# Performance work log

Measured on AMD Instinct MI355X. Metric: run time of the kernel, lower is better.

The kernel has to match this reference:

```python
import jax, jax.numpy as jnp
import numpy as np

# Static multi-level feature-map geometry (h, w) per level.
SPATIAL_SHAPES = np.array([[92, 92], [46, 46], [23, 23], [12, 12]], dtype=np.int32)
_AREAS = SPATIAL_SHAPES[:, 0] * SPATIAL_SHAPES[:, 1]
LEVEL_START = np.concatenate([[0], np.cumsum(_AREAS)[:-1]]).astype(np.int32)
LEN_IN = int(_AREAS.sum())  # 11253
N_HEADS, N_LEVELS, N_POINTS = 8, 4, 4
D_MODEL, D_HEAD = 256, 64


def setup_inputs() -> dict:
    key = jax.random.key(0)
    ks = jax.random.split(key, 12)
    N, Lq = 4, 1000
    s = 0.02
    f32 = jnp.float32
    return {
        'query': jax.random.normal(ks[0], (N, Lq, D_MODEL), f32),
        'reference_points': jax.random.uniform(ks[1], (N, Lq, N_LEVELS, 2), f32),
        'input_flatten': jax.random.normal(ks[2], (N, LEN_IN, D_MODEL), f32),
        'input_spatial_shapes': jnp.asarray(SPATIAL_SHAPES),
        'input_level_start_index': jnp.asarray(LEVEL_START),
        'W_off': jax.random.normal(ks[3], (N_HEADS * N_LEVELS * N_POINTS * 2, D_MODEL), f32) * s,
        'b_off': jax.random.normal(ks[4], (N_HEADS * N_LEVELS * N_POINTS * 2,), f32) * 0.5,
        'W_attn': jax.random.normal(ks[5], (N_HEADS * N_LEVELS * N_POINTS, D_MODEL), f32) * s,
        'b_attn': jax.random.normal(ks[6], (N_HEADS * N_LEVELS * N_POINTS,), f32) * s,
        'W_val': jax.random.normal(ks[7], (N_HEADS * D_HEAD, D_MODEL), f32) * s,
        'b_val': jnp.zeros((N_HEADS * D_HEAD,), f32),
        'W_out': jax.random.normal(ks[8], (D_MODEL, N_HEADS * D_HEAD), f32) * s,
        'b_out': jnp.zeros((D_MODEL,), f32),
    }


def _ms_deform_attn(value, sampling_locations, attention_weights):
    # value: [N, Len_in, H, D]; locations: [N, Lq, H, L, P, 2] in [0,1];
    # weights: [N, Lq, H, L, P] -> out [N, Lq, H*D]
    N, _, H, D = value.shape
    Lq, L, P = sampling_locations.shape[1], sampling_locations.shape[3], sampling_locations.shape[4]
    out = jnp.zeros((N, H, Lq, D), value.dtype)
    for l in range(L):
        h, w = int(SPATIAL_SHAPES[l, 0]), int(SPATIAL_SHAPES[l, 1])
        st = int(LEVEL_START[l])
        # per-level value as [N*H, h*w, D]
        v = value[:, st:st + h * w].transpose(0, 2, 1, 3).reshape(N * H, h * w, D)
        loc = sampling_locations[:, :, :, l].transpose(0, 2, 1, 3, 4).reshape(N * H, Lq * P, 2)
        aw = attention_weights[:, :, :, l].transpose(0, 2, 1, 3).reshape(N * H, Lq * P)
        # grid_sample align_corners=False convention (matches CUDA kernel)
        x = loc[..., 0] * w - 0.5
        y = loc[..., 1] * h - 0.5
        x0 = jnp.floor(x)
        y0 = jnp.floor(y)
        lx, ly = x - x0, y - y0
        x0i = x0.astype(jnp.int32)
        y0i = y0.astype(jnp.int32)

        def gather(yi, xi):
            valid = ((xi >= 0) & (xi < w) & (yi >= 0) & (yi < h)).astype(v.dtype)
            idx = jnp.clip(yi, 0, h - 1) * w + jnp.clip(xi, 0, w - 1)
            g = jnp.take_along_axis(v, idx[..., None], axis=1)  # [N*H, Lq*P, D]
            return g * valid[..., None]

        sampled = (gather(y0i, x0i) * ((1 - lx) * (1 - ly))[..., None]
                   + gather(y0i, x0i + 1) * (lx * (1 - ly))[..., None]
                   + gather(y0i + 1, x0i) * ((1 - lx) * ly)[..., None]
                   + gather(y0i + 1, x0i + 1) * (lx * ly)[..., None])
        out = out + (sampled * aw[..., None]).reshape(N, H, Lq, P, D).sum(axis=3)
    return out.transpose(0, 2, 1, 3).reshape(N, Lq, H * D)


def reference(query, reference_points, input_flatten, input_spatial_shapes,
              input_level_start_index, W_off, b_off, W_attn, b_attn,
              W_val, b_val, W_out, b_out):
    N, Lq, _ = query.shape
    Lin = input_flatten.shape[1]
    H, L, P, D = N_HEADS, N_LEVELS, N_POINTS, D_HEAD
    value = (input_flatten @ W_val.T + b_val).reshape(N, Lin, H, D)
    off = (query @ W_off.T + b_off).reshape(N, Lq, H, L, P, 2)
    aw = jax.nn.softmax((query @ W_attn.T + b_attn).reshape(N, Lq, H, L * P), axis=-1)
    aw = aw.reshape(N, Lq, H, L, P)
    # offset normalizer is (w, h) per level
    norm = jnp.asarray(SPATIAL_SHAPES[:, ::-1].copy(), jnp.float32)  # [L, 2]
    loc = reference_points[:, :, None, :, None, :] + off / norm[None, None, None, :, None, :]
    out = _ms_deform_attn(value, loc, aw)
    return out @ W_out.T + b_out
```

## Files before the change

### kernel.cpp

```cpp
#include <hip/hip_runtime.h>


typedef __attribute__((ext_vector_type(4))) float f32x4;
typedef __attribute__((ext_vector_type(8))) short bf16x8;
typedef __attribute__((ext_vector_type(4))) short bf16x4;

static __device__ __forceinline__ unsigned short f2bf(float f) {
    unsigned u = __builtin_bit_cast(unsigned, f);
    u += 0x7FFFu + ((u >> 16) & 1u);
    return (unsigned short)(u >> 16);
}
static __device__ __forceinline__ float bflo(unsigned d) {
    return __builtin_bit_cast(float, d << 16);
}
static __device__ __forceinline__ float bfhi(unsigned d) {
    return __builtin_bit_cast(float, d & 0xffff0000u);
}
static __device__ __forceinline__ void gload_lds16(const void* g, void* l) {
    __builtin_amdgcn_global_load_lds(
        (const __attribute__((address_space(1))) void*)g,
        (__attribute__((address_space(3))) void*)l, 16, 0, 0);
}

__global__ __launch_bounds__(256)
void cvt_k(const float* __restrict__ s0, const float* __restrict__ s1,
           const float* __restrict__ s2, const float* __restrict__ s3,
           const float* __restrict__ s4, const float* __restrict__ s5,
           unsigned short* __restrict__ dst) {
    const size_t i8 = ((size_t)blockIdx.x * 256 + threadIdx.x) * 8;
    if (i8 >= 12907520u) return;
    const float* sp; size_t loc;
    if (i8 < 11523072u)      { sp = s0; loc = i8; }
    else if (i8 < 12547072u) { sp = s1; loc = i8 - 11523072u; }
    else if (i8 < 12612608u) { sp = s2; loc = i8 - 12547072u; }
    else if (i8 < 12645376u) { sp = s3; loc = i8 - 12612608u; }
    else if (i8 < 12776448u) { sp = s4; loc = i8 - 12645376u; }
    else                     { sp = s5; loc = i8 - 12776448u; }
    f32x4 a = *(const f32x4*)(sp + loc);
    f32x4 b = *(const f32x4*)(sp + loc + 4);
    bf16x8 r;
    r[0] = f2bf(a[0]); r[1] = f2bf(a[1]); r[2] = f2bf(a[2]); r[3] = f2bf(a[3]);
    r[4] = f2bf(b[0]); r[5] = f2bf(b[1]); r[6] = f2bf(b[2]); r[7] = f2bf(b[3]);
    *(bf16x8*)(dst + i8) = r;
}

template<int MODE>
__global__ __launch_bounds__(256)
void gemm_bf16_tn(const unsigned short* __restrict__ A,
                  const unsigned short* __restrict__ B,
                  const float* __restrict__ bias, const float* __restrict__ bias2,
                  void* __restrict__ Cv, int M, int N, int K) {
    __shared__ __align__(16) char smem[65536];

    const int tid = threadIdx.x, lane = tid & 63, w = tid >> 6;
    const int wm = w >> 1, wn = w & 1;
    const int bm = blockIdx.x, bn = blockIdx.y;

    const int r8 = lane >> 3;
    const int colsrc = (((lane & 7) ^ r8) << 4);
    const char* pa[4]; const char* pb[4];
#pragma unroll
    for (int j = 0; j < 4; j++) {
        int ra = bm * 128 + j * 32 + w * 8 + r8; ra = ra < M ? ra : M - 1;
        int rb = bn * 128 + j * 32 + w * 8 + r8; rb = rb < N ? rb : N - 1;
        pa[j] = (const char*)A + (size_t)ra * ((size_t)K * 2) + colsrc;
        pb[j] = (const char*)B + (size_t)rb * ((size_t)K * 2) + colsrc;
    }
    const int ldso = w << 10;
    const int NT = K >> 6;

    f32x4 acc[4][4] = {};
    const int fr = lane & 15, fq = lane >> 4;
    const int k8b = fq << 4;
    const int swzR = (fr & 7) << 4;

#pragma unroll
    for (int j = 0; j < 4; j++) {
        gload_lds16(pa[j], smem + j * 4096 + ldso);
        gload_lds16(pb[j], smem + 16384 + j * 4096 + ldso);
    }
    __syncthreads();

    for (int t = 0; t < NT; ++t) {
        const int cur = (t & 1) << 15;
        if (t + 1 < NT) {
            const int nxt = ((t + 1) & 1) << 15;
            const int off = (t + 1) << 7;
#pragma unroll
            for (int j = 0; j < 4; j++) {
                gload_lds16(pa[j] + off, smem + nxt + j * 4096 + ldso);
                gload_lds16(pb[j] + off, smem + nxt + 16384 + j * 4096 + ldso);
            }
        }
#pragma unroll
        for (int kk = 0; kk < 2; ++kk) {
            const int ko = ((kk << 6) + k8b) ^ swzR;
            bf16x8 af[4], bv[4];
#pragma unroll
            for (int m = 0; m < 4; m++)
                af[m] = *(const bf16x8*)(smem + cur + ((wm * 64 + m * 16 + fr) << 7) + ko);
#pragma unroll
            for (int nn = 0; nn < 4; nn++)
                bv[nn] = *(const bf16x8*)(smem + cur + 16384 + ((wn * 64 + nn * 16 + fr) << 7) + ko);
#pragma unroll
            for (int m = 0; m < 4; m++)
#pragma unroll
                for (int nn = 0; nn < 4; nn++)
                    acc[m][nn] = __builtin_amdgcn_mfma_f32_16x16x32_bf16(
                        af[m], bv[nn], acc[m][nn], 0, 0, 0);
        }
        __syncthreads();
    }

    if (MODE != 1) {
        float* C = (float*)Cv;
        const int crow0 = bm * 128 + wm * 64 + fq * 4;
        const int ccol0 = bn * 128 + wn * 64 + fr;
#pragma unroll
        for (int m = 0; m < 4; m++) {
#pragma unroll
            for (int nn = 0; nn < 4; nn++) {
                const int col = ccol0 + nn * 16;
                const float bv2 = (MODE == 2 && col >= 256) ? bias2[col - 256]
                                                            : bias[col];
#pragma unroll
                for (int j = 0; j < 4; j++) {
                    const int row = crow0 + m * 16 + j;
                    if (row < M) C[(size_t)row * N + col] = acc[m][nn][j] + bv2;
                }
            }
        }
    } else {
        unsigned short* tile = (unsigned short*)smem + (size_t)w * (64 * 68);
        const int hh = bn * 2 + wn;
        float bvs[4];
#pragma unroll
        for (int nn = 0; nn < 4; nn++) bvs[nn] = bias[hh * 64 + nn * 16 + fr];
#pragma unroll
        for (int m = 0; m < 4; m++)
#pragma unroll
            for (int nn = 0; nn < 4; nn++)
#pragma unroll
                for (int j = 0; j < 4; j++)
                    tile[(m * 16 + fq * 4 + j) * 68 + nn * 16 + fr] =
                        f2bf(acc[m][nn][j] + bvs[nn]);
        __syncthreads();
        unsigned short* VT = (unsigned short*)Cv;
        const int q4 = (lane & 15) * 4;
        const int prow = lane >> 4;
#pragma unroll
        for (int it = 0; it < 16; ++it) {
            const int pl = it * 4 + prow;
            const int pixg = bm * 128 + wm * 64 + pl;
            if (pixg < M) {
                const int n = pixg / 11253;
                const int pix = pixg - n * 11253;
                bf16x4 v = *(const bf16x4*)&tile[pl * 68 + q4];
                *(bf16x4*)(VT + ((size_t)(n * 8 + hh) * 11253 + pix) * 64 + q4) = v;
            }
        }
    }
}

__global__ __launch_bounds__(256)
void sample_k(const unsigned short* __restrict__ valueT,
              const float* __restrict__ refp,
              const float* __restrict__ fused,
              unsigned int* __restrict__ msout)
{
    const int bid = blockIdx.x;
    const int xcd = bid & 7;
    const int jj  = bid >> 3;
    const int sl  = jj / 250;
    const int qb  = jj - sl * 250;
    const int nh  = xcd * 4 + sl;
    const int q   = __builtin_amdgcn_readfirstlane(qb * 4 + (threadIdx.x >> 6));
    const int lane = threadIdx.x & 63;
    const int g    = lane >> 5;
    const int n = nh >> 3, h = nh & 7;
    const int nq = n * 1000 + q;

    const float* lgp = fused + (size_t)nq * 384 + 256 + h * 16;
    float mx = lgp[0];
#pragma unroll
    for (int pp = 1; pp < 16; pp++) mx = fmaxf(mx, lgp[pp]);
    float s = 0.f;
#pragma unroll
    for (int pp = 0; pp < 16; pp++) s += __expf(lgp[pp] - mx);

    const int p  = lane & 15;
    const int lv = p >> 2;
    const int W  = lv == 0 ? 92 : lv == 1 ? 46 : lv == 2 ? 23 : 12;
    const int st = lv == 0 ? 0 : lv == 1 ? 8464 : lv == 2 ? 10580 : 11109;

    const float a  = __expf(lgp[p] - mx) / s;
    const float rx = refp[(size_t)nq * 8 + lv * 2 + 0];
    const float ry = refp[(size_t)nq * 8 + lv * 2 + 1];
    const float ox = fused[(size_t)nq * 384 + h * 32 + p * 2 + 0];
    const float oy = fused[(size_t)nq * 384 + h * 32 + p * 2 + 1];

    const float x = rx * (float)W + ox - 0.5f;
    const float y = ry * (float)W + oy - 0.5f;
    const float xf = floorf(x), yf = floorf(y);
    const int x0 = (int)xf, y0 = (int)yf;
    const float lx = x - xf, ly = y - yf;
    const int xb = min(max(x0, 0), W - 2);
    const int yb = min(max(y0, 0), W - 2);
    const float wx0 = (xb     == x0) ? (1.f - lx) : ((xb     == x0 + 1) ? lx : 0.f);
    const float wx1 = (xb + 1 == x0) ? (1.f - lx) : ((xb + 1 == x0 + 1) ? lx : 0.f);
    const float wy0 = (yb     == y0) ? (1.f - ly) : ((yb     == y0 + 1) ? ly : 0.f);
    const float wy1 = (yb + 1 == y0) ? (1.f - ly) : ((yb + 1 == y0 + 1) ? ly : 0.f);
    const int idx0v = st + yb * W + xb;
    const int idx1v = idx0v + W;
    const float wxs = (lane & 16) ? wx1 : wx0;
    const float wav = a * wxs * wy0;
    const float wbv = a * wxs * wy1;

    const unsigned int* vb =
        (const unsigned int*)valueT + (size_t)nh * 11253 * 32;

    float acc0 = 0.f, acc1 = 0.f;
    const int srcb = g << 4;
#pragma unroll
    for (int pp = 0; pp < 16; pp++) {
        const int src = pp + srcb;
        const int   i0 = __shfl(idx0v, src);
        const int   i1 = __shfl(idx1v, src);
        const float w0 = __shfl(wav,   src);
        const float w1 = __shfl(wbv,   src);
        const unsigned d0 = vb[i0 * 32 + lane];
        const unsigned d1 = vb[i1 * 32 + lane];
        acc0 = fmaf(w0, bflo(d0), acc0);
        acc1 = fmaf(w0, bfhi(d0), acc1);
        acc0 = fmaf(w1, bflo(d1), acc0);
        acc1 = fmaf(w1, bfhi(d1), acc1);
    }

    acc0 += __shfl(acc0, lane ^ 32);
    acc1 += __shfl(acc1, lane ^ 32);
    if (lane < 32) {
        const unsigned u = (unsigned)f2bf(acc0) | ((unsigned)f2bf(acc1) << 16);
        msout[(size_t)nq * 256 + h * 32 + (lane & 31)] = u;
    }
}

extern "C" void kernel_launch(void* const* d_in, const int* in_sizes, int n_in,
                              void* d_out, int out_size, void* d_ws, size_t ws_size,
                              hipStream_t stream) {
    (void)in_sizes; (void)n_in; (void)out_size; (void)ws_size;

    const float* query  = (const float*)d_in[0];
    const float* refp   = (const float*)d_in[1];
    const float* inpf   = (const float*)d_in[2];
    const float* W_off  = (const float*)d_in[5];
    const float* b_off  = (const float*)d_in[6];
    const float* W_attn = (const float*)d_in[7];
    const float* b_attn = (const float*)d_in[8];
    const float* W_val  = (const float*)d_in[9];
    const float* b_val  = (const float*)d_in[10];
    const float* W_out  = (const float*)d_in[11];
    const float* b_out  = (const float*)d_in[12];
    float* out = (float*)d_out;

    char* ws = (char*)d_ws;
    unsigned short* bf = (unsigned short*)ws;
    unsigned short* inpfb   = bf;
    unsigned short* queryb  = bf + 11523072;
    unsigned short* W_offb  = bf + 12547072;
    unsigned short* W_valb  = bf + 12645376;
    unsigned short* W_outb  = bf + 12776448;
    unsigned short* valueT  = (unsigned short*)(ws + 25815040);
    float* fusedb = (float*)(ws + 71907328);
    unsigned int* msoutu = (unsigned int*)(ws + 78051328);
    unsigned short* msoutb = (unsigned short*)msoutu;

    cvt_k<<<6303, 256, 0, stream>>>(inpf, query, W_off, W_attn, W_val, W_out, bf);
    gemm_bf16_tn<1><<<dim3(352, 4), 256, 0, stream>>>(
        inpfb, W_valb, b_val, nullptr, valueT, 45012, 512, 256);
    gemm_bf16_tn<2><<<dim3(32, 3), 256, 0, stream>>>(
        queryb, W_offb, b_off, b_attn, fusedb, 4000, 384, 256);
    sample_k<<<8000, 256, 0, stream>>>(valueT, refp, fusedb, msoutu);
    gemm_bf16_tn<0><<<dim3(32, 2), 256, 0, stream>>>(
        msoutb, W_outb, b_out, nullptr, out, 4000, 256, 512);
}
```

Baseline: 95.91 us.

## Fuse fp32-to-bf16 conversion into GEMM tile loads, drop separate convert kernel

Removes the standalone conversion kernel that wrote bf16 copies of the input, query and weights. The GEMMs now stage fp32 tiles into LDS and convert to bf16 with packed convert instructions just before the MFMAs. This saves one launch and a full extra read/write pass over the large input tensor. In exchange it doubles LDS tile size and LDS read traffic for fp32 operands, which can lower occupancy and add conversion ALU work inside the main loop.

```diff
diff --git a/kernel.cpp b/kernel.cpp
--- a/kernel.cpp
+++ b/kernel.cpp
@@ -2,6 +2,7 @@
 
 
 typedef __attribute__((ext_vector_type(4))) float f32x4;
+typedef __attribute__((ext_vector_type(4))) unsigned int u32x4;
 typedef __attribute__((ext_vector_type(8))) short bf16x8;
 typedef __attribute__((ext_vector_type(4))) short bf16x4;
 
@@ -16,98 +17,124 @@
 static __device__ __forceinline__ float bfhi(unsigned d) {
     return __builtin_bit_cast(float, d & 0xffff0000u);
 }
+static __device__ __forceinline__ unsigned cvtpk(float lo, float hi) {
+    unsigned r;
+    asm("v_cvt_pk_bf16_f32 %0, %1, %2" : "=v"(r) : "v"(lo), "v"(hi));
+    return r;
+}
 static __device__ __forceinline__ void gload_lds16(const void* g, void* l) {
     __builtin_amdgcn_global_load_lds(
         (const __attribute__((address_space(1))) void*)g,
         (__attribute__((address_space(3))) void*)l, 16, 0, 0);
 }
 
+template<int MODE, int AF32>
 __global__ __launch_bounds__(256)
-void cvt_k(const float* __restrict__ s0, const float* __restrict__ s1,
-           const float* __restrict__ s2, const float* __restrict__ s3,
-           const float* __restrict__ s4, const float* __restrict__ s5,
-           unsigned short* __restrict__ dst) {
-    const size_t i8 = ((size_t)blockIdx.x * 256 + threadIdx.x) * 8;
-    if (i8 >= 12907520u) return;
-    const float* sp; size_t loc;
-    if (i8 < 11523072u)      { sp = s0; loc = i8; }
-    else if (i8 < 12547072u) { sp = s1; loc = i8 - 11523072u; }
-    else if (i8 < 12612608u) { sp = s2; loc = i8 - 12547072u; }
-    else if (i8 < 12645376u) { sp = s3; loc = i8 - 12612608u; }
-    else if (i8 < 12776448u) { sp = s4; loc = i8 - 12645376u; }
-    else                     { sp = s5; loc = i8 - 12776448u; }
-    f32x4 a = *(const f32x4*)(sp + loc);
-    f32x4 b = *(const f32x4*)(sp + loc + 4);
-    bf16x8 r;
-    r[0] = f2bf(a[0]); r[1] = f2bf(a[1]); r[2] = f2bf(a[2]); r[3] = f2bf(a[3]);
-    r[4] = f2bf(b[0]); r[5] = f2bf(b[1]); r[6] = f2bf(b[2]); r[7] = f2bf(b[3]);
-    *(bf16x8*)(dst + i8) = r;
-}
-
-template<int MODE>
-__global__ __launch_bounds__(256)
-void gemm_bf16_tn(const unsigned short* __restrict__ A,
-                  const unsigned short* __restrict__ B,
-                  const float* __restrict__ bias, const float* __restrict__ bias2,
-                  void* __restrict__ Cv, int M, int N, int K) {
-    __shared__ __align__(16) char smem[65536];
+void gemm_k(const void* __restrict__ Av, const void* __restrict__ Bv,
+            const void* __restrict__ B2v,
+            const float* __restrict__ bias, const float* __restrict__ bias2,
+            void* __restrict__ Cv, int M, int N, int K) {
+    constexpr int APH = AF32 ? 32768 : 16384;
+    constexpr int PH  = APH + 32768;
+    __shared__ __align__(16) char smem[2 * PH];
 
     const int tid = threadIdx.x, lane = tid & 63, w = tid >> 6;
     const int wm = w >> 1, wn = w & 1;
     const int bm = blockIdx.x, bn = blockIdx.y;
-
+    const int rlow = tid >> 4;
+    const int cs32 = (((tid & 15) ^ (rlow & 7)) << 4);
     const int r8 = lane >> 3;
-    const int colsrc = (((lane & 7) ^ r8) << 4);
-    const char* pa[4]; const char* pb[4];
-#pragma unroll
-    for (int j = 0; j < 4; j++) {
-        int ra = bm * 128 + j * 32 + w * 8 + r8; ra = ra < M ? ra : M - 1;
-        int rb = bn * 128 + j * 32 + w * 8 + r8; rb = rb < N ? rb : N - 1;
-        pa[j] = (const char*)A + (size_t)ra * ((size_t)K * 2) + colsrc;
-        pb[j] = (const char*)B + (size_t)rb * ((size_t)K * 2) + colsrc;
-    }
-    const int ldso = w << 10;
+    const int cs16 = (((lane & 7) ^ r8) << 4);
+
+    const char* pa[8];
+    if (AF32) {
+#pragma unroll
+        for (int j = 0; j < 8; j++) {
+            int ra = bm * 128 + j * 16 + rlow; ra = ra < M ? ra : M - 1;
+            pa[j] = (const char*)Av + (size_t)ra * ((size_t)K * 4) + cs32;
+        }
+    } else {
+#pragma unroll
+        for (int j = 0; j < 4; j++) {
+            int ra = bm * 128 + j * 32 + w * 8 + r8; ra = ra < M ? ra : M - 1;
+            pa[j] = (const char*)Av + (size_t)ra * ((size_t)K * 2) + cs16;
+        }
+    }
+    const char* pb[8];
+#pragma unroll
+    for (int j = 0; j < 8; j++) {
+        int rb = bn * 128 + j * 16 + rlow; rb = rb < N ? rb : N - 1;
+        const char* bs = (const char*)Bv;
+        if (MODE == 2 && rb >= 256) { bs = (const char*)B2v; rb -= 256; }
+        pb[j] = bs + (size_t)rb * ((size_t)K * 4) + cs32;
+    }
+
+    const int wofs = w << 10;
     const int NT = K >> 6;
-
     f32x4 acc[4][4] = {};
-    const int fr = lane & 15, fq = lane >> 4;
-    const int k8b = fq << 4;
-    const int swzR = (fr & 7) << 4;
-
-#pragma unroll
-    for (int j = 0; j < 4; j++) {
-        gload_lds16(pa[j], smem + j * 4096 + ldso);
-        gload_lds16(pb[j], smem + 16384 + j * 4096 + ldso);
-    }
+    const int fr = lane & 15, fq = lane >> 4, fr7 = fr & 7;
+
+    auto stageA = [&](int t, char* base) {
+        if (AF32) {
+            const int o = t << 8;
+#pragma unroll
+            for (int j = 0; j < 8; j++) gload_lds16(pa[j] + o, base + j * 4096 + wofs);
+        } else {
+            const int o = t << 7;
+#pragma unroll
+            for (int j = 0; j < 4; j++) gload_lds16(pa[j] + o, base + j * 4096 + wofs);
+        }
+    };
+    auto stageB = [&](int t, char* base) {
+        const int o = t << 8;
+#pragma unroll
+        for (int j = 0; j < 8; j++) gload_lds16(pb[j] + o, base + j * 4096 + wofs);
+    };
+
+    stageA(0, smem); stageB(0, smem + APH);
     __syncthreads();
 
     for (int t = 0; t < NT; ++t) {
-        const int cur = (t & 1) << 15;
+        char* cur = smem + (size_t)(t & 1) * PH;
         if (t + 1 < NT) {
-            const int nxt = ((t + 1) & 1) << 15;
-            const int off = (t + 1) << 7;
-#pragma unroll
-            for (int j = 0; j < 4; j++) {
-                gload_lds16(pa[j] + off, smem + nxt + j * 4096 + ldso);
-                gload_lds16(pb[j] + off, smem + nxt + 16384 + j * 4096 + ldso);
+            char* nxt = smem + (size_t)((t + 1) & 1) * PH;
+            stageA(t + 1, nxt); stageB(t + 1, nxt + APH);
+        }
+#pragma unroll
+        for (int kk = 0; kk < 2; ++kk) {
+            bf16x8 af[4], bfv[4];
+            if (AF32) {
+#pragma unroll
+                for (int m = 0; m < 4; m++) {
+                    const char* rp = cur + ((wm * 64 + m * 16 + fr) << 8);
+                    f32x4 x0 = *(const f32x4*)(rp + ((((kk << 3) + (fq << 1) + 0) ^ fr7) << 4));
+                    f32x4 x1 = *(const f32x4*)(rp + ((((kk << 3) + (fq << 1) + 1) ^ fr7) << 4));
+                    u32x4 u = { cvtpk(x0[0], x0[1]), cvtpk(x0[2], x0[3]),
+                                cvtpk(x1[0], x1[1]), cvtpk(x1[2], x1[3]) };
+                    af[m] = __builtin_bit_cast(bf16x8, u);
+                }
+            } else {
+                const int ko = ((kk << 6) + (fq << 4)) ^ (fr7 << 4);
+#pragma unroll
+                for (int m = 0; m < 4; m++)
+                    af[m] = *(const bf16x8*)(cur + ((wm * 64 + m * 16 + fr) << 7) + ko);
             }
-        }
-#pragma unroll
-        for (int kk = 0; kk < 2; ++kk) {
-            const int ko = ((kk << 6) + k8b) ^ swzR;
-            bf16x8 af[4], bv[4];
-#pragma unroll
-            for (int m = 0; m < 4; m++)
-                af[m] = *(const bf16x8*)(smem + cur + ((wm * 64 + m * 16 + fr) << 7) + ko);
-#pragma unroll
-            for (int nn = 0; nn < 4; nn++)
-                bv[nn] = *(const bf16x8*)(smem + cur + 16384 + ((wn * 64 + nn * 16 + fr) << 7) + ko);
+            const char* bb = cur + APH;
+#pragma unroll
+            for (int nn = 0; nn < 4; nn++) {
+                const char* rp = bb + ((wn * 64 + nn * 16 + fr) << 8);
+                f32x4 x0 = *(const f32x4*)(rp + ((((kk << 3) + (fq << 1) + 0) ^ fr7) << 4));
+                f32x4 x1 = *(const f32x4*)(rp + ((((kk << 3) + (fq << 1) + 1) ^ fr7) << 4));
+                u32x4 u = { cvtpk(x0[0], x0[1]), cvtpk(x0[2], x0[3]),
+                            cvtpk(x1[0], x1[1]), cvtpk(x1[2], x1[3]) };
+                bfv[nn] = __builtin_bit_cast(bf16x8, u);
+            }
 #pragma unroll
             for (int m = 0; m < 4; m++)
 #pragma unroll
                 for (int nn = 0; nn < 4; nn++)
                     acc[m][nn] = __builtin_amdgcn_mfma_f32_16x16x32_bf16(
-                        af[m], bv[nn], acc[m][nn], 0, 0, 0);
+                        af[m], bfv[nn], acc[m][nn], 0, 0, 0);
         }
         __syncthreads();
     }
@@ -263,23 +290,16 @@
     float* out = (float*)d_out;
 
     char* ws = (char*)d_ws;
-    unsigned short* bf = (unsigned short*)ws;
-    unsigned short* inpfb   = bf;
-    unsigned short* queryb  = bf + 11523072;
-    unsigned short* W_offb  = bf + 12547072;
-    unsigned short* W_valb  = bf + 12645376;
-    unsigned short* W_outb  = bf + 12776448;
-    unsigned short* valueT  = (unsigned short*)(ws + 25815040);
-    float* fusedb = (float*)(ws + 71907328);
-    unsigned int* msoutu = (unsigned int*)(ws + 78051328);
+    unsigned short* valueT = (unsigned short*)ws;
+    float* fusedb = (float*)(ws + 46092288);
+    unsigned int* msoutu = (unsigned int*)(ws + 52236288);
     unsigned short* msoutb = (unsigned short*)msoutu;
 
-    cvt_k<<<6303, 256, 0, stream>>>(inpf, query, W_off, W_attn, W_val, W_out, bf);
-    gemm_bf16_tn<1><<<dim3(352, 4), 256, 0, stream>>>(
-        inpfb, W_valb, b_val, nullptr, valueT, 45012, 512, 256);
-    gemm_bf16_tn<2><<<dim3(32, 3), 256, 0, stream>>>(
-        queryb, W_offb, b_off, b_attn, fusedb, 4000, 384, 256);
+    gemm_k<1, 1><<<dim3(352, 4), 256, 0, stream>>>(
+        inpf, W_val, nullptr, b_val, nullptr, valueT, 45012, 512, 256);
+    gemm_k<2, 1><<<dim3(32, 3), 256, 0, stream>>>(
+        query, W_off, W_attn, b_off, b_attn, fusedb, 4000, 384, 256);
     sample_k<<<8000, 256, 0, stream>>>(valueT, refp, fusedb, msoutu);
-    gemm_bf16_tn<0><<<dim3(32, 2), 256, 0, stream>>>(
-        msoutb, W_outb, b_out, nullptr, out, 4000, 256, 512);
-}
+    gemm_k<0, 0><<<dim3(32, 2), 256, 0, stream>>>(
+        msoutb, W_out, nullptr, b_out, nullptr, out, 4000, 256, 512);
+}
```

Result: slower. 115.6 us (+20.5%).
